# Performance work log

Hardware: AMD Instinct MI355X
Metric: run time of the kernel (lower is better)

Reference implementation:

```python
import jax, jax.numpy as jnp
import numpy as np

B, S, H, E, V = 64, 2048, 1024, 512, 32000


def setup_inputs() -> dict:
    key = jax.random.key(0)
    ks = jax.random.split(key, 10)
    s = lambda k, shape, scale: jax.random.normal(k, shape, jnp.float32) * scale
    return {
        "input_batch": jax.random.randint(ks[0], (B,), 0, V),
        "prev_h": s(ks[1], (B, H), 0.1),
        "prev_c": s(ks[2], (B, H), 0.1),
        "encoder_outputs": s(ks[3], (S, B, H), 0.1),
        "emb_W": s(ks[4], (V, E), 0.02),           # nn.Embedding weight
        "attn_W": s(ks[5], (2 * H,), 0.02),        # nn.Linear(2H, 1) weight (flattened)
        "attn_b": jnp.zeros((), jnp.float32),
        "W_ih": s(ks[6], (4 * H, E + H), 0.02),    # LSTMCell weight_ih
        "W_hh": s(ks[7], (4 * H, H), 0.02),        # LSTMCell weight_hh
        "b_ih": jnp.zeros((4 * H,), jnp.float32),
        "b_hh": jnp.zeros((4 * H,), jnp.float32),
        "out_W": s(ks[8], (V, H), 0.02),           # linear_out weight
        "out_b": jnp.zeros((V,), jnp.float32),
    }


def reference(input_batch, prev_h, prev_c, encoder_outputs, emb_W, attn_W, attn_b,
              W_ih, W_hh, b_ih, b_hh, out_W, out_b):
    hid = prev_h.shape[1]
    emb = emb_W[input_batch]                                   # [B, E]

    # Additive attention score attn(cat(prev_h[i], enc[j,i])) vectorized:
    # score[b, s] = prev_h[b] . W[:H] + enc[s, b] . W[H:] + bias
    Wh, We = attn_W[:hid], attn_W[hid:]
    scores = (prev_h @ Wh)[:, None] + jnp.einsum("sbh,h->bs", encoder_outputs, We) + attn_b
    attn_weights = jax.nn.softmax(scores, axis=1)              # [B, S]

    # context = bmm(attn[B,1,S], enc^T[B,S,H]) -> [B, H]
    context = jnp.einsum("bs,sbh->bh", attn_weights, encoder_outputs)

    x = jnp.concatenate([emb, context], axis=1)                # [B, E+H]

    # LSTMCell step (PyTorch gate order: i, f, g, o)
    gates = x @ W_ih.T + b_ih + prev_h @ W_hh.T + b_hh         # [B, 4H]
    i, f, g, o = jnp.split(gates, 4, axis=1)
    i, f, o = jax.nn.sigmoid(i), jax.nn.sigmoid(f), jax.nn.sigmoid(o)
    g = jnp.tanh(g)
    cell = f * prev_c + i * g
    hidden = o * jnp.tanh(cell)

    logits = hidden @ out_W.T + out_b                          # [B, V]
    output = jax.nn.log_softmax(logits, axis=1)
    return output, hidden, cell, attn_weights
```

## Files before the change

kernel.cpp:

```cpp
#include <hip/hip_runtime.h>
#include <math.h>

#define B 64
#define S 2048
#define H 1024
#define E 512
#define V 32000
#define G4 4096
#define KX 1536
#define KC 2560
#define NVT 500

typedef __attribute__((ext_vector_type(8))) short short8v;
typedef __attribute__((ext_vector_type(4))) float f32x4;

__device__ __forceinline__ ushort f2bf(float f) {
    union { float f; unsigned u; } v; v.f = f;
    unsigned r = v.u + 0x7FFFu + ((v.u >> 16) & 1u);
    return (ushort)(r >> 16);
}

__device__ __forceinline__ float4 ntload4(const float* p) {
    f32x4 v = __builtin_nontemporal_load((const f32x4*)p);
    return make_float4(v[0], v[1], v[2], v[3]);
}

__global__ __launch_bounds__(256, 4) void fused_attn_kernel(const float* __restrict__ enc,
                                                            const float* __restrict__ attn_W,
                                                            const float* __restrict__ attn_b,
                                                            const float* __restrict__ prev_h,
                                                            float* __restrict__ scores,
                                                            float* __restrict__ cpart,
                                                            float* __restrict__ mlc) {
    __shared__ float red[256];
    __shared__ float mw[4], lw[4];
    __shared__ float cbuf[4][1024];
    int t = threadIdx.x;
    int lane = t & 63, wid = t >> 6;
    int b = blockIdx.x >> 4, cpair = blockIdx.x & 15;

    {
        float4 p = *(const float4*)(prev_h + b * H + t * 4);
        float4 w = *(const float4*)(attn_W + t * 4);
        red[t] = p.x * w.x + p.y * w.y + p.z * w.z + p.w * w.w;
        __syncthreads();
        for (int s2 = 128; s2; s2 >>= 1) {
            if (t < s2) red[t] += red[t + s2];
            __syncthreads();
        }
    }
    float cst = red[0] + attn_b[0];

    const float* We = attn_W + H;
    float4 we4[4];
#pragma unroll
    for (int c = 0; c < 4; ++c) we4[c] = *(const float4*)(We + c * 256 + lane * 4);

    float m = -INFINITY, l = 0.f;
    float4 ctx4[4] = {{0,0,0,0},{0,0,0,0},{0,0,0,0},{0,0,0,0}};

    for (int cc = 0; cc < 2; ++cc) {
        int chunk = cpair * 2 + cc;
        int s0 = chunk * 64 + wid * 16;
        const float* rowp = enc + (size_t)s0 * (B * H) + b * H + lane * 4;
        float4 e4[4];
#pragma unroll
        for (int c = 0; c < 4; ++c) e4[c] = ntload4(rowp + c * 256);

        for (int i = 0; i < 16; ++i) {
            float4 cur[4];
#pragma unroll
            for (int c = 0; c < 4; ++c) cur[c] = e4[c];
            if (i < 15) {
                const float* np = rowp + (size_t)(i + 1) * (B * H);
#pragma unroll
                for (int c = 0; c < 4; ++c) e4[c] = ntload4(np + c * 256);
            }
            float acc = 0.f;
#pragma unroll
            for (int c = 0; c < 4; ++c)
                acc += cur[c].x * we4[c].x + cur[c].y * we4[c].y +
                       cur[c].z * we4[c].z + cur[c].w * we4[c].w;
#pragma unroll
            for (int x = 32; x; x >>= 1) acc += __shfl_xor(acc, x);
            float score = acc + cst;
            if (lane == 0) scores[b * S + s0 + i] = score;
            float nm = fmaxf(m, score);
            float sc = expf(m - nm);
            float w = expf(score - nm);
            l = l * sc + w;
            m = nm;
#pragma unroll
            for (int c = 0; c < 4; ++c) {
                ctx4[c].x = ctx4[c].x * sc + w * cur[c].x;
                ctx4[c].y = ctx4[c].y * sc + w * cur[c].y;
                ctx4[c].z = ctx4[c].z * sc + w * cur[c].z;
                ctx4[c].w = ctx4[c].w * sc + w * cur[c].w;
            }
        }
    }

    if (lane == 0) { mw[wid] = m; lw[wid] = l; }
    __syncthreads();
    float M = fmaxf(fmaxf(mw[0], mw[1]), fmaxf(mw[2], mw[3]));
    float L = lw[0] * expf(mw[0] - M) + lw[1] * expf(mw[1] - M) +
              lw[2] * expf(mw[2] - M) + lw[3] * expf(mw[3] - M);
    float msc = expf(m - M);
#pragma unroll
    for (int c = 0; c < 4; ++c) {
        float4 v = ctx4[c];
        v.x *= msc; v.y *= msc; v.z *= msc; v.w *= msc;
        *(float4*)&cbuf[wid][c * 256 + lane * 4] = v;
    }
    __syncthreads();
    if (wid == 0) {
#pragma unroll
        for (int c = 0; c < 4; ++c) {
            int h = c * 256 + lane * 4;
            float4 a0 = *(float4*)&cbuf[0][h];
            float4 a1 = *(float4*)&cbuf[1][h];
            float4 a2 = *(float4*)&cbuf[2][h];
            float4 a3 = *(float4*)&cbuf[3][h];
            float4 s4 = make_float4(a0.x + a1.x + a2.x + a3.x,
                                    a0.y + a1.y + a2.y + a3.y,
                                    a0.z + a1.z + a2.z + a3.z,
                                    a0.w + a1.w + a2.w + a3.w);
            *(float4*)(cpart + (size_t)(cpair * B + b) * H + h) = s4;
        }
    }
    if (t == 0) {
        mlc[(b * 16 + cpair) * 2] = M;
        mlc[(b * 16 + cpair) * 2 + 1] = L;
    }
}

__global__ __launch_bounds__(256) void attn_reduce_kernel(const float* __restrict__ cpart,
                                                          const float* __restrict__ mlc,
                                                          const float* __restrict__ scores,
                                                          const int* __restrict__ ib,
                                                          const float* __restrict__ emb_W,
                                                          const float* __restrict__ prev_h,
                                                          ushort* __restrict__ xb,
                                                          float* __restrict__ attn) {
    __shared__ float Ms[16], Ls[16], Es[16];
    int blk = blockIdx.x;
    int b = blk >> 2, q = blk & 3;
    int t = threadIdx.x;
    if (t < 16) {
        Ms[t] = mlc[(b * 16 + t) * 2];
        Ls[t] = mlc[(b * 16 + t) * 2 + 1];
    }
    __syncthreads();
    float Mg = -INFINITY;
#pragma unroll
    for (int c = 0; c < 16; ++c) Mg = fmaxf(Mg, Ms[c]);
    if (t < 16) Es[t] = expf(Ms[t] - Mg);
    __syncthreads();
    float Lg = 0.f;
#pragma unroll
    for (int c = 0; c < 16; ++c) Lg += Ls[c] * Es[c];
    float inv = 1.f / Lg;
    int h = q * 256 + t;
    float acc = 0.f;
#pragma unroll 4
    for (int c = 0; c < 16; ++c)
        acc += Es[c] * cpart[(size_t)(c * B + b) * H + h];
    xb[(size_t)b * KC + E + h] = f2bf(acc * inv);
#pragma unroll
    for (int i = 0; i < 2; ++i) {
        int s = q * 512 + i * 256 + t;
        attn[b * S + s] = expf(scores[b * S + s] - Mg) * inv;
    }
#pragma unroll
    for (int i = 0; i < 2; ++i) {
        int j = q * 384 + i * 256 + t;
        if (i == 1 && t >= 128) break;
        if (j < E) xb[(size_t)b * KC + j] = f2bf(emb_W[(size_t)ib[b] * E + j]);
        else       xb[(size_t)b * KC + KX + (j - E)] = f2bf(prev_h[b * H + (j - E)]);
    }
}

__global__ __launch_bounds__(256) void gates_mfma(const float* __restrict__ W_ih,
                                                  const float* __restrict__ W_hh,
                                                  const ushort* __restrict__ xb,
                                                  float* __restrict__ gpart) {
    __shared__ ushort Wt[64 * 64];
    __shared__ ushort Bt[64 * 64];
    int t = threadIdx.x;
    int lane = t & 63, wid = t >> 6;
    int rtile = blockIdx.x >> 3, ks = blockIdx.x & 7;
    int r0 = rtile * 64;

    int srow = t >> 2;
    int sq = t & 3;

    f32x4 acc[4] = {{0.f,0.f,0.f,0.f},{0.f,0.f,0.f,0.f},{0.f,0.f,0.f,0.f},{0.f,0.f,0.f,0.f}};

    int r = lane & 15, g = lane >> 4;
    int arow = wid * 16 + r;
    int aswz = (arow & 7) << 4;
    unsigned abase = arow * 128;

    for (int kt = 0; kt < 5; ++kt) {
        int kb = ks * 320 + kt * 64;
        const float* wbase;
        int wstride;
        if (kb < KX) { wbase = W_ih + kb; wstride = KX; }
        else         { wbase = W_hh + (kb - KX); wstride = H; }
        __syncthreads();
        {
            const float* src = wbase + (size_t)(r0 + srow) * wstride + sq * 16;
            float4 f0 = ntload4(src + 0);
            float4 f1 = ntload4(src + 4);
            float4 f2 = ntload4(src + 8);
            float4 f3 = ntload4(src + 12);
            short8v w0, w1;
            w0[0] = (short)f2bf(f0.x); w0[1] = (short)f2bf(f0.y);
            w0[2] = (short)f2bf(f0.z); w0[3] = (short)f2bf(f0.w);
            w0[4] = (short)f2bf(f1.x); w0[5] = (short)f2bf(f1.y);
            w0[6] = (short)f2bf(f1.z); w0[7] = (short)f2bf(f1.w);
            w1[0] = (short)f2bf(f2.x); w1[1] = (short)f2bf(f2.y);
            w1[2] = (short)f2bf(f2.z); w1[3] = (short)f2bf(f2.w);
            w1[4] = (short)f2bf(f3.x); w1[5] = (short)f2bf(f3.y);
            w1[6] = (short)f2bf(f3.z); w1[7] = (short)f2bf(f3.w);
            unsigned rb = srow * 128;
            unsigned sw = (srow & 7) << 4;
            *(short8v*)((char*)Wt + rb + ((sq * 32 + 0) ^ sw))  = w0;
            *(short8v*)((char*)Wt + rb + ((sq * 32 + 16) ^ sw)) = w1;
        }
        {
            const ushort* hsrc = xb + (size_t)srow * KC + kb + sq * 16;
            uint4 h0 = *(const uint4*)(hsrc);
            uint4 h1 = *(const uint4*)(hsrc + 8);
            unsigned rb = srow * 128;
            unsigned sw = (srow & 7) << 4;
            *(uint4*)((char*)Bt + rb + ((sq * 32 + 0) ^ sw))  = h0;
            *(uint4*)((char*)Bt + rb + ((sq * 32 + 16) ^ sw)) = h1;
        }
        __syncthreads();
#pragma unroll
        for (int kk = 0; kk < 2; ++kk) {
            unsigned koff = kk * 64 + g * 16;
            short8v a = *(short8v*)((char*)Wt + abase + (koff ^ aswz));
#pragma unroll
            for (int bt = 0; bt < 4; ++bt) {
                int brow = bt * 16 + r;
                short8v bb = *(short8v*)((char*)Bt + brow * 128 + (koff ^ ((brow & 7) << 4)));
                acc[bt] = __builtin_amdgcn_mfma_f32_16x16x32_bf16(a, bb, acc[bt], 0, 0, 0);
            }
        }
    }
#pragma unroll
    for (int bt = 0; bt < 4; ++bt) {
        int bcol = bt * 16 + r;
#pragma unroll
        for (int j = 0; j < 4; ++j) {
            int rg = r0 + wid * 16 + g * 4 + j;
            gpart[(size_t)ks * (G4 * B) + (size_t)rg * B + bcol] = acc[bt][j];
        }
    }
}

__global__ __launch_bounds__(256) void lstm_kernel(const float* __restrict__ gpart,
                                                   const float* __restrict__ b_ih,
                                                   const float* __restrict__ b_hh,
                                                   const float* __restrict__ prev_c,
                                                   float* __restrict__ hidden_out,
                                                   float* __restrict__ cell_out,
                                                   ushort* __restrict__ hb) {
    int t = blockIdx.x * 256 + threadIdx.x;
    int b = t & 63, h = t >> 6;
    float g[4];
#pragma unroll
    for (int q = 0; q < 4; ++q) {
        int r = h + q * H;
        float a = b_ih[r] + b_hh[r];
#pragma unroll
        for (int ks = 0; ks < 8; ++ks) a += gpart[(size_t)ks * (G4 * B) + r * B + b];
        g[q] = a;
    }
    float ig = 1.f / (1.f + expf(-g[0]));
    float fg = 1.f / (1.f + expf(-g[1]));
    float gg = tanhf(g[2]);
    float og = 1.f / (1.f + expf(-g[3]));
    float c = fg * prev_c[b * H + h] + ig * gg;
    float hd = og * tanhf(c);
    cell_out[b * H + h] = c;
    hidden_out[b * H + h] = hd;
    hb[b * H + h] = f2bf(hd);
}

__global__ __launch_bounds__(256) void logits_mfma(const float* __restrict__ W,
                                                   const float* __restrict__ ob,
                                                   const ushort* __restrict__ hb,
                                                   float* __restrict__ outl,
                                                   float* __restrict__ lsp) {
    __shared__ ushort Wt[64 * 64];
    __shared__ ushort Bt[64 * 64];
    __shared__ float  Ct[64][68];
    int t = threadIdx.x;
    int lane = t & 63, wid = t >> 6;
    int v0 = blockIdx.x * 64;

    int srow = t >> 2;
    int sq = t & 3;

    f32x4 acc[4] = {{0.f,0.f,0.f,0.f},{0.f,0.f,0.f,0.f},{0.f,0.f,0.f,0.f},{0.f,0.f,0.f,0.f}};

    int r = lane & 15, g = lane >> 4;
    int arow = wid * 16 + r;
    int aswz = (arow & 7) << 4;
    unsigned abase = arow * 128;

    for (int kt = 0; kt < 16; ++kt) {
        int k0 = kt * 64;
        __syncthreads();
        {
            const float* src = W + (size_t)(v0 + srow) * H + k0 + sq * 16;
            float4 f0 = ntload4(src + 0);
            float4 f1 = ntload4(src + 4);
            float4 f2 = ntload4(src + 8);
            float4 f3 = ntload4(src + 12);
            short8v w0, w1;
            w0[0] = (short)f2bf(f0.x); w0[1] = (short)f2bf(f0.y);
            w0[2] = (short)f2bf(f0.z); w0[3] = (short)f2bf(f0.w);
            w0[4] = (short)f2bf(f1.x); w0[5] = (short)f2bf(f1.y);
            w0[6] = (short)f2bf(f1.z); w0[7] = (short)f2bf(f1.w);
            w1[0] = (short)f2bf(f2.x); w1[1] = (short)f2bf(f2.y);
            w1[2] = (short)f2bf(f2.z); w1[3] = (short)f2bf(f2.w);
            w1[4] = (short)f2bf(f3.x); w1[5] = (short)f2bf(f3.y);
            w1[6] = (short)f2bf(f3.z); w1[7] = (short)f2bf(f3.w);
            unsigned rb = srow * 128;
            unsigned sw = (srow & 7) << 4;
            *(short8v*)((char*)Wt + rb + ((sq * 32 + 0) ^ sw))  = w0;
            *(short8v*)((char*)Wt + rb + ((sq * 32 + 16) ^ sw)) = w1;
        }
        {
            const ushort* hsrc = hb + (size_t)srow * H + k0 + sq * 16;
            uint4 h0 = *(const uint4*)(hsrc);
            uint4 h1 = *(const uint4*)(hsrc + 8);
            unsigned rb = srow * 128;
            unsigned sw = (srow & 7) << 4;
            *(uint4*)((char*)Bt + rb + ((sq * 32 + 0) ^ sw))  = h0;
            *(uint4*)((char*)Bt + rb + ((sq * 32 + 16) ^ sw)) = h1;
        }
        __syncthreads();
#pragma unroll
        for (int kk = 0; kk < 2; ++kk) {
            unsigned koff = kk * 64 + g * 16;
            short8v a = *(short8v*)((char*)Wt + abase + (koff ^ aswz));
#pragma unroll
            for (int bt = 0; bt < 4; ++bt) {
                int brow = bt * 16 + r;
                short8v bb = *(short8v*)((char*)Bt + brow * 128 + (koff ^ ((brow & 7) << 4)));
                acc[bt] = __builtin_amdgcn_mfma_f32_16x16x32_bf16(a, bb, acc[bt], 0, 0, 0);
            }
        }
    }
    __syncthreads();
    float bias[4];
#pragma unroll
    for (int j = 0; j < 4; ++j) bias[j] = ob[v0 + wid * 16 + g * 4 + j];
#pragma unroll
    for (int bt = 0; bt < 4; ++bt)
#pragma unroll
        for (int j = 0; j < 4; ++j)
            Ct[bt * 16 + r][wid * 16 + g * 4 + j] = acc[bt][j] + bias[j];
    __syncthreads();
    int ob_ = t >> 2;
    int vq = (t & 3) * 16;
    float4 vals[4];
    float pm = -3.4e38f;
#pragma unroll
    for (int c = 0; c < 4; ++c) {
        vals[c] = *(float4*)&Ct[ob_][vq + c * 4];
        pm = fmaxf(pm, fmaxf(fmaxf(vals[c].x, vals[c].y), fmaxf(vals[c].z, vals[c].w)));
        *(float4*)(outl + (size_t)ob_ * V + v0 + vq + c * 4) = vals[c];
    }
    float ps = 0.f;
#pragma unroll
    for (int c = 0; c < 4; ++c)
        ps += expf(vals[c].x - pm) + expf(vals[c].y - pm) +
              expf(vals[c].z - pm) + expf(vals[c].w - pm);
#pragma unroll
    for (int x = 1; x <= 2; x <<= 1) {
        float om = __shfl_xor(pm, x);
        float os = __shfl_xor(ps, x);
        float nm = fmaxf(pm, om);
        ps = ps * expf(pm - nm) + os * expf(om - nm);
        pm = nm;
    }
    if ((t & 3) == 0) {
        lsp[((size_t)ob_ * NVT + blockIdx.x) * 2]     = pm;
        lsp[((size_t)ob_ * NVT + blockIdx.x) * 2 + 1] = ps;
    }
}

__global__ __launch_bounds__(256) void lsub_kernel(const float* __restrict__ lsp,
                                                   float* __restrict__ lg) {
    __shared__ float rm[256], rl[256];
    int blk = blockIdx.x;
    int b = blk >> 5, chunk = blk & 31;
    int t = threadIdx.x;
    const float* pb = lsp + (size_t)b * (NVT * 2);
    float m = pb[t * 2], l = pb[t * 2 + 1];
    int i2 = t + 256;
    if (i2 < NVT) {
        float m1 = pb[i2 * 2], l1 = pb[i2 * 2 + 1];
        float nm = fmaxf(m, m1);
        l = l * expf(m - nm) + l1 * expf(m1 - nm);
        m = nm;
    }
    rm[t] = m; rl[t] = l; __syncthreads();
    for (int s2 = 128; s2; s2 >>= 1) {
        if (t < s2) {
            float m2 = rm[t + s2], l2 = rl[t + s2];
            float nm = fmaxf(rm[t], m2);
            rl[t] = rl[t] * expf(rm[t] - nm) + l2 * expf(m2 - nm);
            rm[t] = nm;
        }
        __syncthreads();
    }
    float c = rm[0] + logf(rl[0]);
    if (t < 250) {
        float4* p = (float4*)(lg + (size_t)b * V + chunk * 1000) + t;
        float4 x = *p;
        x.x -= c; x.y -= c; x.z -= c; x.w -= c;
        *p = x;
    }
}

extern "C" void kernel_launch(void* const* d_in, const int* in_sizes, int n_in,
                              void* d_out, int out_size, void* d_ws, size_t ws_size,
                              hipStream_t stream) {
    const int*   ib      = (const int*)d_in[0];
    const float* prev_h  = (const float*)d_in[1];
    const float* prev_c  = (const float*)d_in[2];
    const float* enc     = (const float*)d_in[3];
    const float* emb_W   = (const float*)d_in[4];
    const float* attn_W  = (const float*)d_in[5];
    const float* attn_b  = (const float*)d_in[6];
    const float* W_ih    = (const float*)d_in[7];
    const float* W_hh    = (const float*)d_in[8];
    const float* b_ih    = (const float*)d_in[9];
    const float* b_hh    = (const float*)d_in[10];
    const float* out_W   = (const float*)d_in[11];
    const float* out_b   = (const float*)d_in[12];

    float* ws = (float*)d_ws;
    float* sc   = ws;
    float* cp   = ws + 131072;
    float* gp   = ws + 1179648;
    float* mlc  = ws + 3276800;
    ushort* xb  = (ushort*)(ws + 3278848);
    ushort* hb  = (ushort*)(ws + 3360768);
    float* lsp  = ws + 3393536;

    float* out    = (float*)d_out;
    float* out_ls = out;
    float* out_h  = out + (size_t)B * V;
    float* out_c  = out_h + (size_t)B * H;
    float* out_a  = out_c + (size_t)B * H;

    hipLaunchKernelGGL(fused_attn_kernel,  dim3(1024), dim3(256), 0, stream, enc, attn_W, attn_b, prev_h, sc, cp, mlc);
    hipLaunchKernelGGL(attn_reduce_kernel, dim3(256),  dim3(256), 0, stream, cp, mlc, sc, ib, emb_W, prev_h, xb, out_a);
    hipLaunchKernelGGL(gates_mfma,         dim3(512),  dim3(256), 0, stream, W_ih, W_hh, xb, gp);
    hipLaunchKernelGGL(lstm_kernel,        dim3(256),  dim3(256), 0, stream, gp, b_ih, b_hh, prev_c, out_h, out_c, hb);
    hipLaunchKernelGGL(logits_mfma,        dim3(NVT),  dim3(256), 0, stream, out_W, out_b, hb, out_ls, lsp);
    hipLaunchKernelGGL(lsub_kernel,        dim3(2048), dim3(256), 0, stream, lsp, out_ls);
}
```

Before: 168.4 us.

## Fuse logits GEMM and log-softmax subtraction into one cooperative kernel

Merges the logits MFMA kernel and the log-softmax normalisation kernel into a single cooperative launch. Grid-wide syncs separate the per-tile partial max/sum stage, a per-row reduction done by 64 blocks, and the final subtraction. The logits stay in registers and are written once, already normalised, which removes the write-then-read-modify-write pass over the 64x32000 output and one kernel launch. In exchange it adds two grid barriers and requires all 512 blocks to be co-resident.

```diff
diff --git a/kernel.cpp b/kernel.cpp
--- a/kernel.cpp
+++ b/kernel.cpp
@@ -1,5 +1,8 @@
 #include <hip/hip_runtime.h>
+#include <hip/hip_cooperative_groups.h>
 #include <math.h>
+
+namespace cg = cooperative_groups;
 
 #define B 64
 #define S 2048
@@ -290,143 +293,153 @@
     hb[b * H + h] = f2bf(hd);
 }
 
-__global__ __launch_bounds__(256) void logits_mfma(const float* __restrict__ W,
-                                                   const float* __restrict__ ob,
-                                                   const ushort* __restrict__ hb,
-                                                   float* __restrict__ outl,
-                                                   float* __restrict__ lsp) {
+__global__ __launch_bounds__(256) void logits_lsub_coop(const float* __restrict__ W,
+                                                        const float* __restrict__ ob,
+                                                        const ushort* __restrict__ hb,
+                                                        float* __restrict__ outl,
+                                                        float* __restrict__ lsp,
+                                                        float* __restrict__ cvec) {
+    cg::grid_group grid = cg::this_grid();
     __shared__ ushort Wt[64 * 64];
     __shared__ ushort Bt[64 * 64];
     __shared__ float  Ct[64][68];
+    __shared__ float  rm[256], rl[256];
     int t = threadIdx.x;
     int lane = t & 63, wid = t >> 6;
     int v0 = blockIdx.x * 64;
-
-    int srow = t >> 2;
-    int sq = t & 3;
-
-    f32x4 acc[4] = {{0.f,0.f,0.f,0.f},{0.f,0.f,0.f,0.f},{0.f,0.f,0.f,0.f},{0.f,0.f,0.f,0.f}};
-
-    int r = lane & 15, g = lane >> 4;
-    int arow = wid * 16 + r;
-    int aswz = (arow & 7) << 4;
-    unsigned abase = arow * 128;
-
-    for (int kt = 0; kt < 16; ++kt) {
-        int k0 = kt * 64;
-        __syncthreads();
-        {
-            const float* src = W + (size_t)(v0 + srow) * H + k0 + sq * 16;
-            float4 f0 = ntload4(src + 0);
-            float4 f1 = ntload4(src + 4);
-            float4 f2 = ntload4(src + 8);
-            float4 f3 = ntload4(src + 12);
-            short8v w0, w1;
-            w0[0] = (short)f2bf(f0.x); w0[1] = (short)f2bf(f0.y);
-            w0[2] = (short)f2bf(f0.z); w0[3] = (short)f2bf(f0.w);
-            w0[4] = (short)f2bf(f1.x); w0[5] = (short)f2bf(f1.y);
-            w0[6] = (short)f2bf(f1.z); w0[7] = (short)f2bf(f1.w);
-            w1[0] = (short)f2bf(f2.x); w1[1] = (short)f2bf(f2.y);
-            w1[2] = (short)f2bf(f2.z); w1[3] = (short)f2bf(f2.w);
-            w1[4] = (short)f2bf(f3.x); w1[5] = (short)f2bf(f3.y);
-            w1[6] = (short)f2bf(f3.z); w1[7] = (short)f2bf(f3.w);
-            unsigned rb = srow * 128;
-            unsigned sw = (srow & 7) << 4;
-            *(short8v*)((char*)Wt + rb + ((sq * 32 + 0) ^ sw))  = w0;
-            *(short8v*)((char*)Wt + rb + ((sq * 32 + 16) ^ sw)) = w1;
-        }
-        {
-            const ushort* hsrc = hb + (size_t)srow * H + k0 + sq * 16;
-            uint4 h0 = *(const uint4*)(hsrc);
-            uint4 h1 = *(const uint4*)(hsrc + 8);
-            unsigned rb = srow * 128;
-            unsigned sw = (srow & 7) << 4;
-            *(uint4*)((char*)Bt + rb + ((sq * 32 + 0) ^ sw))  = h0;
-            *(uint4*)((char*)Bt + rb + ((sq * 32 + 16) ^ sw)) = h1;
-        }
-        __syncthreads();
-#pragma unroll
-        for (int kk = 0; kk < 2; ++kk) {
-            unsigned koff = kk * 64 + g * 16;
-            short8v a = *(short8v*)((char*)Wt + abase + (koff ^ aswz));
-#pragma unroll
-            for (int bt = 0; bt < 4; ++bt) {
-                int brow = bt * 16 + r;
-                short8v bb = *(short8v*)((char*)Bt + brow * 128 + (koff ^ ((brow & 7) << 4)));
-                acc[bt] = __builtin_amdgcn_mfma_f32_16x16x32_bf16(a, bb, acc[bt], 0, 0, 0);
-            }
-        }
-    }
-    __syncthreads();
-    float bias[4];
-#pragma unroll
-    for (int j = 0; j < 4; ++j) bias[j] = ob[v0 + wid * 16 + g * 4 + j];
-#pragma unroll
-    for (int bt = 0; bt < 4; ++bt)
-#pragma unroll
-        for (int j = 0; j < 4; ++j)
-            Ct[bt * 16 + r][wid * 16 + g * 4 + j] = acc[bt][j] + bias[j];
-    __syncthreads();
     int ob_ = t >> 2;
     int vq = (t & 3) * 16;
     float4 vals[4];
-    float pm = -3.4e38f;
-#pragma unroll
-    for (int c = 0; c < 4; ++c) {
-        vals[c] = *(float4*)&Ct[ob_][vq + c * 4];
-        pm = fmaxf(pm, fmaxf(fmaxf(vals[c].x, vals[c].y), fmaxf(vals[c].z, vals[c].w)));
-        *(float4*)(outl + (size_t)ob_ * V + v0 + vq + c * 4) = vals[c];
-    }
-    float ps = 0.f;
-#pragma unroll
-    for (int c = 0; c < 4; ++c)
-        ps += expf(vals[c].x - pm) + expf(vals[c].y - pm) +
-              expf(vals[c].z - pm) + expf(vals[c].w - pm);
-#pragma unroll
-    for (int x = 1; x <= 2; x <<= 1) {
-        float om = __shfl_xor(pm, x);
-        float os = __shfl_xor(ps, x);
-        float nm = fmaxf(pm, om);
-        ps = ps * expf(pm - nm) + os * expf(om - nm);
-        pm = nm;
-    }
-    if ((t & 3) == 0) {
-        lsp[((size_t)ob_ * NVT + blockIdx.x) * 2]     = pm;
-        lsp[((size_t)ob_ * NVT + blockIdx.x) * 2 + 1] = ps;
-    }
-}
-
-__global__ __launch_bounds__(256) void lsub_kernel(const float* __restrict__ lsp,
-                                                   float* __restrict__ lg) {
-    __shared__ float rm[256], rl[256];
-    int blk = blockIdx.x;
-    int b = blk >> 5, chunk = blk & 31;
-    int t = threadIdx.x;
-    const float* pb = lsp + (size_t)b * (NVT * 2);
-    float m = pb[t * 2], l = pb[t * 2 + 1];
-    int i2 = t + 256;
-    if (i2 < NVT) {
-        float m1 = pb[i2 * 2], l1 = pb[i2 * 2 + 1];
-        float nm = fmaxf(m, m1);
-        l = l * expf(m - nm) + l1 * expf(m1 - nm);
-        m = nm;
-    }
-    rm[t] = m; rl[t] = l; __syncthreads();
-    for (int s2 = 128; s2; s2 >>= 1) {
-        if (t < s2) {
-            float m2 = rm[t + s2], l2 = rl[t + s2];
-            float nm = fmaxf(rm[t], m2);
-            rl[t] = rl[t] * expf(rm[t] - nm) + l2 * expf(m2 - nm);
-            rm[t] = nm;
+
+    if (blockIdx.x < NVT) {
+        int srow = t >> 2;
+        int sq = t & 3;
+
+        f32x4 acc[4] = {{0.f,0.f,0.f,0.f},{0.f,0.f,0.f,0.f},{0.f,0.f,0.f,0.f},{0.f,0.f,0.f,0.f}};
+
+        int r = lane & 15, g = lane >> 4;
+        int arow = wid * 16 + r;
+        int aswz = (arow & 7) << 4;
+        unsigned abase = arow * 128;
+
+        for (int kt = 0; kt < 16; ++kt) {
+            int k0 = kt * 64;
+            __syncthreads();
+            {
+                const float* src = W + (size_t)(v0 + srow) * H + k0 + sq * 16;
+                float4 f0 = ntload4(src + 0);
+                float4 f1 = ntload4(src + 4);
+                float4 f2 = ntload4(src + 8);
+                float4 f3 = ntload4(src + 12);
+                short8v w0, w1;
+                w0[0] = (short)f2bf(f0.x); w0[1] = (short)f2bf(f0.y);
+                w0[2] = (short)f2bf(f0.z); w0[3] = (short)f2bf(f0.w);
+                w0[4] = (short)f2bf(f1.x); w0[5] = (short)f2bf(f1.y);
+                w0[6] = (short)f2bf(f1.z); w0[7] = (short)f2bf(f1.w);
+                w1[0] = (short)f2bf(f2.x); w1[1] = (short)f2bf(f2.y);
+                w1[2] = (short)f2bf(f2.z); w1[3] = (short)f2bf(f2.w);
+                w1[4] = (short)f2bf(f3.x); w1[5] = (short)f2bf(f3.y);
+                w1[6] = (short)f2bf(f3.z); w1[7] = (short)f2bf(f3.w);
+                unsigned rb = srow * 128;
+                unsigned sw = (srow & 7) << 4;
+                *(short8v*)((char*)Wt + rb + ((sq * 32 + 0) ^ sw))  = w0;
+                *(short8v*)((char*)Wt + rb + ((sq * 32 + 16) ^ sw)) = w1;
+            }
+            {
+                const ushort* hsrc = hb + (size_t)srow * H + k0 + sq * 16;
+                uint4 h0 = *(const uint4*)(hsrc);
+                uint4 h1 = *(const uint4*)(hsrc + 8);
+                unsigned rb = srow * 128;
+                unsigned sw = (srow & 7) << 4;
+                *(uint4*)((char*)Bt + rb + ((sq * 32 + 0) ^ sw))  = h0;
+                *(uint4*)((char*)Bt + rb + ((sq * 32 + 16) ^ sw)) = h1;
+            }
+            __syncthreads();
+#pragma unroll
+            for (int kk = 0; kk < 2; ++kk) {
+                unsigned koff = kk * 64 + g * 16;
+                short8v a = *(short8v*)((char*)Wt + abase + (koff ^ aswz));
+#pragma unroll
+                for (int bt = 0; bt < 4; ++bt) {
+                    int brow = bt * 16 + r;
+                    short8v bb = *(short8v*)((char*)Bt + brow * 128 + (koff ^ ((brow & 7) << 4)));
+                    acc[bt] = __builtin_amdgcn_mfma_f32_16x16x32_bf16(a, bb, acc[bt], 0, 0, 0);
+                }
+            }
         }
         __syncthreads();
-    }
-    float c = rm[0] + logf(rl[0]);
-    if (t < 250) {
-        float4* p = (float4*)(lg + (size_t)b * V + chunk * 1000) + t;
-        float4 x = *p;
-        x.x -= c; x.y -= c; x.z -= c; x.w -= c;
-        *p = x;
+        float bias[4];
+#pragma unroll
+        for (int j = 0; j < 4; ++j) bias[j] = ob[v0 + wid * 16 + g * 4 + j];
+#pragma unroll
+        for (int bt = 0; bt < 4; ++bt)
+#pragma unroll
+            for (int j = 0; j < 4; ++j)
+                Ct[bt * 16 + r][wid * 16 + g * 4 + j] = acc[bt][j] + bias[j];
+        __syncthreads();
+        float pm = -3.4e38f;
+#pragma unroll
+        for (int c = 0; c < 4; ++c) {
+            vals[c] = *(float4*)&Ct[ob_][vq + c * 4];
+            pm = fmaxf(pm, fmaxf(fmaxf(vals[c].x, vals[c].y), fmaxf(vals[c].z, vals[c].w)));
+        }
+        float ps = 0.f;
+#pragma unroll
+        for (int c = 0; c < 4; ++c)
+            ps += expf(vals[c].x - pm) + expf(vals[c].y - pm) +
+                  expf(vals[c].z - pm) + expf(vals[c].w - pm);
+#pragma unroll
+        for (int x = 1; x <= 2; x <<= 1) {
+            float om = __shfl_xor(pm, x);
+            float os = __shfl_xor(ps, x);
+            float nm = fmaxf(pm, om);
+            ps = ps * expf(pm - nm) + os * expf(om - nm);
+            pm = nm;
+        }
+        if ((t & 3) == 0) {
+            lsp[((size_t)ob_ * NVT + blockIdx.x) * 2]     = pm;
+            lsp[((size_t)ob_ * NVT + blockIdx.x) * 2 + 1] = ps;
+        }
+        __threadfence();
+    }
+
+    grid.sync();
+
+    if (blockIdx.x < 64) {
+        int b = blockIdx.x;
+        const float* pb = lsp + (size_t)b * (NVT * 2);
+        float m = pb[t * 2], l = pb[t * 2 + 1];
+        int i2 = t + 256;
+        if (i2 < NVT) {
+            float m1 = pb[i2 * 2], l1 = pb[i2 * 2 + 1];
+            float nm = fmaxf(m, m1);
+            l = l * expf(m - nm) + l1 * expf(m1 - nm);
+            m = nm;
+        }
+        rm[t] = m; rl[t] = l; __syncthreads();
+        for (int s2 = 128; s2; s2 >>= 1) {
+            if (t < s2) {
+                float m2 = rm[t + s2], l2 = rl[t + s2];
+                float nm = fmaxf(rm[t], m2);
+                rl[t] = rl[t] * expf(rm[t] - nm) + l2 * expf(m2 - nm);
+                rm[t] = nm;
+            }
+            __syncthreads();
+        }
+        if (t == 0) cvec[b] = rm[0] + logf(rl[0]);
+        __threadfence();
+    }
+
+    grid.sync();
+
+    if (blockIdx.x < NVT) {
+        float cc = cvec[ob_];
+#pragma unroll
+        for (int c = 0; c < 4; ++c) {
+            float4 x = vals[c];
+            x.x -= cc; x.y -= cc; x.z -= cc; x.w -= cc;
+            *(float4*)(outl + (size_t)ob_ * V + v0 + vq + c * 4) = x;
+        }
     }
 }
 
@@ -455,6 +468,7 @@
     ushort* xb  = (ushort*)(ws + 3278848);
     ushort* hb  = (ushort*)(ws + 3360768);
     float* lsp  = ws + 3393536;
+    float* cvec = mlc;
 
     float* out    = (float*)d_out;
     float* out_ls = out;
@@ -466,6 +480,8 @@
     hipLaunchKernelGGL(attn_reduce_kernel, dim3(256),  dim3(256), 0, stream, cp, mlc, sc, ib, emb_W, prev_h, xb, out_a);
     hipLaunchKernelGGL(gates_mfma,         dim3(512),  dim3(256), 0, stream, W_ih, W_hh, xb, gp);
     hipLaunchKernelGGL(lstm_kernel,        dim3(256),  dim3(256), 0, stream, gp, b_ih, b_hh, prev_c, out_h, out_c, hb);
-    hipLaunchKernelGGL(logits_mfma,        dim3(NVT),  dim3(256), 0, stream, out_W, out_b, hb, out_ls, lsp);
-    hipLaunchKernelGGL(lsub_kernel,        dim3(2048), dim3(256), 0, stream, lsp, out_ls);
-}
+
+    void* args[] = { (void*)&out_W, (void*)&out_b, (void*)&hb,
+                     (void*)&out_ls, (void*)&lsp, (void*)&cvec };
+    hipLaunchCooperativeKernel((const void*)logits_lsub_coop, dim3(512), dim3(256), args, 0, stream);
+}
```

New measurement: 328.2 us. 1.95x slower.
